# Kernel optimization log

Measured on AMD Instinct MI355X. Metric: run time of the kernel, lower is better.

The kernel has to match this reference:

```python
import jax, jax.numpy as jnp
import numpy as np

B = 512; S = 6; Q = 2            # meta-batch, n_way*k_shot, n_way*q_query
DIM = 64; IMG = 28; N_WAY = 2
HEADS = 4; HD = DIM // HEADS     # retrieval heads / head dim
EPS = 1e-5


def _pool_mat(inp, out):
    # exact torch AdaptiveAvgPool2d windowing as a matrix [out, inp]
    P = np.zeros((out, inp), np.float32)
    for i in range(out):
        s = (i * inp) // out
        e = -((-(i + 1) * inp) // out)
        P[i, s:e] = 1.0 / (e - s)
    return jnp.asarray(P)

P28 = _pool_mat(IMG, 8)  # 28 -> 8; subsequent 8 -> 8 pools are identity


def _gelu(x):
    return jax.nn.gelu(x, approximate=False)


def _conv(x, w, b):
    y = jax.lax.conv_general_dilated(x, w, (1, 1), ((1, 1), (1, 1)),
                                     dimension_numbers=('NCHW', 'OIHW', 'NCHW'))
    return y + b[None, :, None, None]


def _bn(x, p):
    # p rows: gamma, beta, running_mean, running_var (eval-mode BatchNorm2d)
    g, bt, m, v = p[0], p[1], p[2], p[3]
    sc = g / jnp.sqrt(v + EPS)
    return (x - m[None, :, None, None]) * sc[None, :, None, None] + bt[None, :, None, None]


def _img_in(x, c1w, c1b, bn1, c2w, c2b, bn2, c3w, c3b, bn3, c4w, c4b, bn4, lin_w):
    h = _bn(_conv(x, c1w, c1b), bn1)
    h = jnp.einsum('oi,ncij,pj->ncop', P28, h, P28)   # adaptive avg pool 28x28 -> 8x8
    h = _gelu(h)                                       # dropout is identity in eval
    h = _gelu(_bn(_conv(h, c2w, c2b), bn2))
    h = _gelu(_bn(_conv(h, c3w, c3b), bn3))
    h = _gelu(_bn(_conv(h, c4w, c4b), bn4))            # -> [N,1,8,8]
    h = h.reshape(h.shape[0], -1)                      # [N,64]
    return h @ lin_w.T                                 # Linear(64 -> DIM, no bias)


def _net(x, w1, w2):
    # x: [B,K,D]; w1,w2: [B,D,D] batched fast weights
    h = jnp.einsum('bed,bkd->bke', w1, x)
    ah = _gelu(h)
    y = jnp.einsum('bed,bkd->bke', w2, ah)
    return y, h


def _get_lor(x, w1, w2, r_q, r_k, r_v, r_o, ln_w, ln_b):
    b, k, _ = x.shape
    q, _ = _net(x, w1, w2)
    qh = jnp.einsum('nhd,bkd->bknh', r_q, q)
    sc = jnp.einsum('bknh,rnh->bknr', qh, r_k) / (HD ** 0.5)
    p = jax.nn.softmax(sc, axis=-1)
    lor = jnp.einsum('bknr,rnh->bknh', p, r_v).reshape(b, k, DIM)
    lor = jnp.einsum('de,bkd->bke', r_o, lor)
    z = lor + x
    mu = z.mean(-1, keepdims=True)
    var = ((z - mu) ** 2).mean(-1, keepdims=True)
    return (z - mu) / jnp.sqrt(var + EPS) * ln_w + ln_b


def _forward(query_w, sxs, qxs, inner_lr, c1w, c1b, bn1, c2w, c2b, bn2, c3w, c3b, bn3,
             c4w, c4b, bn4, lin_w, emb, w1, w2, tags, r_q, r_k, r_v, r_o, ln_w, ln_b,
             sys, qys):
    b = query_w.shape[0]
    s = sxs.shape[1]
    q = qxs.shape[1]
    feats = lambda im: _img_in(im.reshape(-1, 1, IMG, IMG), c1w, c1b, bn1, c2w, c2b,
                               bn2, c3w, c3b, bn3, c4w, c4b, bn4, lin_w)
    sx = feats(sxs).reshape(b, s, DIM)
    qx = feats(qxs).reshape(b, q, DIM)
    qe = tags[4]
    w1b = jnp.broadcast_to(w1, (b, DIM, DIM))
    w2b = jnp.broadcast_to(w2, (b, DIM, DIM))
    bound = sx + emb[sys]                                          # [B,S,D]
    # all 4 tag variants for all S shots in one vectorized get_lor call
    inp = (bound[:, :, None, :] + tags[:4][None, None]).reshape(b, s * 4, DIM)
    lors = _get_lor(inp, w1b, w2b, r_q, r_k, r_v, r_o, ln_w, ln_b).reshape(b, s, 4, DIM)
    l1s, r1s, l2s, r2s = lors[:, :, 0], lors[:, :, 1], lors[:, :, 2], lors[:, :, 3]
    qw1 = w1[None] + jnp.einsum('bsl,bsr->blr', l1s, r1s)
    qw2 = w2[None] + jnp.einsum('bsl,bsr->blr', l2s, r2s)
    preds, _ = _net(qx + qe, qw1, qw2)                             # [B,Q,D]
    logits = jnp.einsum('ld,bqd->bql', emb, preds).reshape(-1, N_WAY)
    labels = qys.reshape(-1)
    ls = jax.nn.log_softmax(logits)
    task_loss = -jnp.take_along_axis(ls, labels[:, None], axis=1).mean()
    n_correct = (jnp.argmax(logits, axis=1) == labels).sum()
    return task_loss, n_correct, b * q


def setup_inputs() -> dict:
    key = jax.random.key(0)
    ks = jax.random.split(key, 24)
    rn = lambda i, sh, sc=1.0: sc * jax.random.normal(ks[i], sh, jnp.float32)
    def bnp(i, c):
        k0, k1, k2 = jax.random.split(ks[i], 3)
        return jnp.stack([1.0 + 0.1 * jax.random.normal(k0, (c,)),
                          0.1 * jax.random.normal(k1, (c,)),
                          0.1 * jax.random.normal(k2, (c,)),
                          0.5 + jax.random.uniform(jax.random.fold_in(ks[i], 3), (c,))])
    return {
        'query_w': rn(0, (B, DIM)),
        'sxs': rn(1, (B, S, IMG * IMG)),
        'qxs': rn(2, (B, Q, IMG * IMG)),
        'inner_lr': jnp.float32(0.1),
        'c1w': rn(3, (32, 1, 3, 3), 0.3), 'c1b': rn(4, (32,), 0.1), 'bn1': bnp(5, 32),
        'c2w': rn(6, (32, 32, 3, 3), 0.06), 'c2b': rn(7, (32,), 0.1), 'bn2': bnp(8, 32),
        'c3w': rn(9, (32, 32, 3, 3), 0.06), 'c3b': rn(10, (32,), 0.1), 'bn3': bnp(11, 32),
        'c4w': rn(12, (1, 32, 3, 3), 0.06), 'c4b': rn(13, (1,), 0.1), 'bn4': bnp(14, 1),
        'lin_w': rn(15, (DIM, 64), 0.125),
        'emb': rn(16, (N_WAY, DIM), 0.125),
        'w1': rn(17, (DIM, DIM), 0.125),
        'w2': rn(18, (DIM, DIM), 0.125),
        'tags': rn(19, (8, DIM), 0.125),
        'r_q': rn(20, (HEADS, HD, DIM), 0.125),
        'r_k': rn(21, (16, HEADS, HD), 0.25),
        'r_v': rn(22, (16, HEADS, HD), 0.25),
        'r_o': rn(23, (DIM, DIM), 0.125),
        'ln_w': 0.001 * jnp.ones((DIM,), jnp.float32),
        'ln_b': jnp.zeros((DIM,), jnp.float32),
        'sys': jax.random.randint(jax.random.fold_in(key, 100), (B, S), 0, N_WAY),
        'qys': jax.random.randint(jax.random.fold_in(key, 101), (B, Q), 0, N_WAY),
    }


def reference(query_w, sxs, qxs, inner_lr, c1w, c1b, bn1, c2w, c2b, bn2, c3w, c3b, bn3,
              c4w, c4b, bn4, lin_w, emb, w1, w2, tags, r_q, r_k, r_v, r_o, ln_w, ln_b,
              sys, qys):
    task_loss, n_correct, n_q = _forward(query_w, sxs, qxs, inner_lr, c1w, c1b, bn1,
                                         c2w, c2b, bn2, c3w, c3b, bn3, c4w, c4b, bn4,
                                         lin_w, emb, w1, w2, tags, r_q, r_k, r_v, r_o,
                                         ln_w, ln_b, sys, qys)
    return (task_loss, task_loss, jnp.float32(0.0), n_correct, n_q)
```

## Files before the change

kernel.cpp:

```cpp
#include <hip/hip_runtime.h>
#include <math.h>

constexpr int NSUP = 3072;
constexpr float EPSF = 1e-5f;

constexpr int WS_W1B  = 0;
constexpr int WS_B1   = 1024;
constexpr int WS_W2B  = 1056;
constexpr int WS_W3B  = 5664;
constexpr int WS_W4B  = 10272;
constexpr int WS_B4   = 10416;
constexpr int WS_B2   = 10420;
constexpr int WS_B3   = 10452;
constexpr int WS_HW1  = 10484;
constexpr int WS_HW2  = 12788;
constexpr int WS_HRQ  = 15092;
constexpr int WS_HROT = 17396;
constexpr int WS_PART = 19700;
constexpr int WS_FEATS= 20724;

using short8 = __attribute__((ext_vector_type(8))) short;
using f32x4  = __attribute__((ext_vector_type(4))) float;

__device__ __forceinline__ float gelu_f(float x) {
    return 0.5f * x * (1.0f + erff(x * 0.70710678118654752440f));
}
__device__ __forceinline__ unsigned short f2bf(float f) {
    unsigned u = __float_as_uint(f);
    return (unsigned short)((u + 0x7FFFu + ((u >> 16) & 1u)) >> 16);
}
__device__ __forceinline__ float bflo(unsigned u) { return __uint_as_float(u << 16); }
__device__ __forceinline__ float bfhi(unsigned u) { return __uint_as_float(u & 0xffff0000u); }

__global__ void __launch_bounds__(256) precompute_kernel(
    const float* __restrict__ c1w, const float* __restrict__ c1b, const float* __restrict__ bn1,
    const float* __restrict__ c2w, const float* __restrict__ c2b, const float* __restrict__ bn2,
    const float* __restrict__ c3w, const float* __restrict__ c3b, const float* __restrict__ bn3,
    const float* __restrict__ c4w, const float* __restrict__ c4b, const float* __restrict__ bn4,
    const float* __restrict__ w1, const float* __restrict__ w2,
    const float* __restrict__ rq, const float* __restrict__ ro,
    float* __restrict__ ws)
{
    const int gid = blockIdx.x * 256 + threadIdx.x;
    const int gsz = gridDim.x * 256;

    unsigned short* w1b = (unsigned short*)(ws + WS_W1B);
    for (int v = gid; v < 2048; v += gsz) {
        int kt = v >> 10, rem = v & 1023, oc = rem >> 5, kk = rem & 31;
        int tap = kt * 32 + kk;
        unsigned short o = 0;
        if (tap < 36) {
            int tt = tap / 6, s = tap - tt * 6;
            float sum = 0.f;
            for (int di = 0; di < 3; ++di) {
                int a = tt - di; if (a < 0 || a > 3) continue;
                for (int dj = 0; dj < 3; ++dj) {
                    int bb = s - dj; if (bb < 0 || bb > 3) continue;
                    sum += c1w[oc * 9 + di * 3 + dj];
                }
            }
            float sc1 = bn1[oc] * rsqrtf(bn1[96 + oc] + EPSF);
            o = f2bf(sum * sc1 * (1.0f / 16.0f));
        }
        w1b[v] = o;
    }
    for (int c = gid; c < 32; c += gsz) {
        float sc1 = bn1[c] * rsqrtf(bn1[96 + c] + EPSF);
        ws[WS_B1 + c] = (c1b[c] - bn1[64 + c]) * sc1 + bn1[32 + c];
        float sc2 = bn2[c] * rsqrtf(bn2[96 + c] + EPSF);
        ws[WS_B2 + c] = (c2b[c] - bn2[64 + c]) * sc2 + bn2[32 + c];
        float sc3 = bn3[c] * rsqrtf(bn3[96 + c] + EPSF);
        ws[WS_B3 + c] = (c3b[c] - bn3[64 + c]) * sc3 + bn3[32 + c];
    }
    unsigned short* w2b = (unsigned short*)(ws + WS_W2B);
    unsigned short* w3b = (unsigned short*)(ws + WS_W3B);
    for (int v = gid; v < 9216; v += gsz) {
        int tap = v >> 10, oc = (v >> 5) & 31, ic = v & 31;
        float sc2 = bn2[oc] * rsqrtf(bn2[96 + oc] + EPSF);
        float sc3 = bn3[oc] * rsqrtf(bn3[96 + oc] + EPSF);
        w2b[v] = f2bf(c2w[oc * 288 + ic * 9 + tap] * sc2);
        w3b[v] = f2bf(c3w[oc * 288 + ic * 9 + tap] * sc3);
    }
    {
        unsigned short* w4b = (unsigned short*)(ws + WS_W4B);
        float sc4 = bn4[0] * rsqrtf(bn4[3] + EPSF);
        for (int v = gid; v < 288; v += gsz) {
            int tap = v >> 5, ic = v & 31;
            w4b[v] = f2bf(c4w[ic * 9 + tap] * sc4);
        }
        if (gid == 0) ws[WS_B4] = (c4b[0] - bn4[2]) * sc4 + bn4[1];
    }
    unsigned short* hw1 = (unsigned short*)(ws + WS_HW1);
    unsigned short* hw2 = (unsigned short*)(ws + WS_HW2);
    unsigned short* hrq = (unsigned short*)(ws + WS_HRQ);
    unsigned short* hro = (unsigned short*)(ws + WS_HROT);
    for (int v = gid; v < 4608; v += gsz) {
        int e = v / 72, d = v - e * 72;
        unsigned short a = 0, b = 0, c = 0, r = 0;
        if (d < 64) {
            a = f2bf(w1[e * 64 + d]);
            b = f2bf(w2[e * 64 + d]);
            c = f2bf(rq[e * 64 + d]);
            r = f2bf(ro[d * 64 + e]);
        }
        hw1[v] = a; hw2[v] = b; hrq[v] = c; hro[v] = r;
    }
}

__global__ void __launch_bounds__(512, 4) feats_kernel(
    const float* __restrict__ sxs, const float* __restrict__ qxs,
    const float* __restrict__ lin_w, const float* __restrict__ ws,
    float* __restrict__ feats)
{
    __shared__ __align__(16) unsigned short sAct[8][3200];
    __shared__ __align__(16) unsigned short sWB[9216];
    __shared__ __align__(16) float sh4[8][64];

    const int t    = threadIdx.x;
    const int wv   = t >> 6;
    const int lane = t & 63;
    const int col  = lane & 15;
    const int quad = lane >> 4;
    const int n    = blockIdx.x * 8 + wv;

    unsigned short* A = sAct[wv];

    {
        uint4 z = {0, 0, 0, 0};
        for (int i = t; i < 3200; i += 512) ((uint4*)sAct)[i] = z;
        if (t < 256) ((uint4*)sWB)[t] = ((const uint4*)(ws + WS_W1B))[t];
    }
    __syncthreads();

    {
        const float* img = (n < NSUP) ? (sxs + (size_t)n * 784) : (qxs + (size_t)(n - NSUP) * 784);
        int ttj[8], ssj[8];
        #pragma unroll
        for (int j = 0; j < 8; ++j) {
            int k = quad * 8 + j;
            ttj[j] = k / 6; ssj[j] = k - ttj[j] * 6;
        }
        f32x4 acc[4][2];
        #pragma unroll
        for (int mt = 0; mt < 4; ++mt) { acc[mt][0] = (f32x4){0,0,0,0}; acc[mt][1] = (f32x4){0,0,0,0}; }

        short8 b00 = *(const short8*)(sWB + (0 * 32 + 0 * 16 + col) * 32 + quad * 8);
        short8 b01 = *(const short8*)(sWB + (0 * 32 + 1 * 16 + col) * 32 + quad * 8);
        short8 b10 = *(const short8*)(sWB + (1 * 32 + 0 * 16 + col) * 32 + quad * 8);
        short8 b11 = *(const short8*)(sWB + (1 * 32 + 1 * 16 + col) * 32 + quad * 8);

        #pragma unroll
        for (int mt = 0; mt < 4; ++mt) {
            int px = mt * 16 + col;
            int sr = (((px >> 3) * 7) >> 1) - 1;
            int sc = (((px & 7) * 7) >> 1) - 1;
            short8 a0;
            #pragma unroll
            for (int j = 0; j < 8; ++j) {
                int rr = sr + ttj[j], cc = sc + ssj[j];
                float v = ((unsigned)rr < 28u && (unsigned)cc < 28u) ? img[rr * 28 + cc] : 0.f;
                a0[j] = (short)f2bf(v);
            }
            acc[mt][0] = __builtin_amdgcn_mfma_f32_16x16x32_bf16(a0, b00, acc[mt][0], 0, 0, 0);
            acc[mt][1] = __builtin_amdgcn_mfma_f32_16x16x32_bf16(a0, b01, acc[mt][1], 0, 0, 0);
            short8 a1 = {0,0,0,0,0,0,0,0};
            if (quad == 0) {
                #pragma unroll
                for (int j = 0; j < 4; ++j) {
                    int rr = sr + 5, cc = sc + 2 + j;
                    float v = ((unsigned)rr < 28u && (unsigned)cc < 28u) ? img[rr * 28 + cc] : 0.f;
                    a1[j] = (short)f2bf(v);
                }
            }
            acc[mt][0] = __builtin_amdgcn_mfma_f32_16x16x32_bf16(a1, b10, acc[mt][0], 0, 0, 0);
            acc[mt][1] = __builtin_amdgcn_mfma_f32_16x16x32_bf16(a1, b11, acc[mt][1], 0, 0, 0);
        }
        float bi0 = ws[WS_B1 + col], bi1 = ws[WS_B1 + 16 + col];
        #pragma unroll
        for (int mt = 0; mt < 4; ++mt)
            #pragma unroll
            for (int reg = 0; reg < 4; ++reg) {
                int px = mt * 16 + quad * 4 + reg;
                unsigned short* dst = A + (((px >> 3) + 1) * 10 + (px & 7) + 1) * 32;
                dst[col]      = f2bf(gelu_f(acc[mt][0][reg] + bi0));
                dst[col + 16] = f2bf(gelu_f(acc[mt][1][reg] + bi1));
            }
    }
    __syncthreads();
    for (int i = t; i < 1152; i += 512) ((uint4*)sWB)[i] = ((const uint4*)(ws + WS_W2B))[i];
    __syncthreads();

    #pragma unroll 1
    for (int layer = 0; layer < 2; ++layer) {
        f32x4 acc[4][2];
        #pragma unroll
        for (int mt = 0; mt < 4; ++mt) { acc[mt][0] = (f32x4){0,0,0,0}; acc[mt][1] = (f32x4){0,0,0,0}; }
        const unsigned short* abase[4];
        #pragma unroll
        for (int mt = 0; mt < 4; ++mt) {
            int px = mt * 16 + col;
            abase[mt] = A + ((px >> 3) * 10 + (px & 7)) * 32 + quad * 8;
        }
        #pragma unroll
        for (int dr = 0; dr < 3; ++dr)
            #pragma unroll
            for (int dc = 0; dc < 3; ++dc) {
                int tap = dr * 3 + dc;
                short8 b0 = *(const short8*)(sWB + (tap * 32 + col) * 32 + quad * 8);
                short8 b1 = *(const short8*)(sWB + (tap * 32 + 16 + col) * 32 + quad * 8);
                #pragma unroll
                for (int mt = 0; mt < 4; ++mt) {
                    short8 a = *(const short8*)(abase[mt] + (dr * 10 + dc) * 32);
                    acc[mt][0] = __builtin_amdgcn_mfma_f32_16x16x32_bf16(a, b0, acc[mt][0], 0, 0, 0);
                    acc[mt][1] = __builtin_amdgcn_mfma_f32_16x16x32_bf16(a, b1, acc[mt][1], 0, 0, 0);
                }
            }
        float bi0 = ws[(layer ? WS_B3 : WS_B2) + col];
        float bi1 = ws[(layer ? WS_B3 : WS_B2) + 16 + col];
        #pragma unroll
        for (int mt = 0; mt < 4; ++mt)
            #pragma unroll
            for (int reg = 0; reg < 4; ++reg) {
                int px = mt * 16 + quad * 4 + reg;
                unsigned short* dst = A + (((px >> 3) + 1) * 10 + (px & 7) + 1) * 32;
                dst[col]      = f2bf(gelu_f(acc[mt][0][reg] + bi0));
                dst[col + 16] = f2bf(gelu_f(acc[mt][1][reg] + bi1));
            }
        __syncthreads();
        if (layer == 0) {
            for (int i = t; i < 1152; i += 512) ((uint4*)sWB)[i] = ((const uint4*)(ws + WS_W3B))[i];
            __syncthreads();
        }
    }

    {
        f32x4 acc4[4];
        #pragma unroll
        for (int mt = 0; mt < 4; ++mt) acc4[mt] = (f32x4){0,0,0,0};
        const unsigned short* abase[4];
        #pragma unroll
        for (int mt = 0; mt < 4; ++mt) {
            int px = mt * 16 + col;
            abase[mt] = A + ((px >> 3) * 10 + (px & 7)) * 32 + quad * 8;
        }
        const unsigned short* w4g = (const unsigned short*)(ws + WS_W4B);
        #pragma unroll
        for (int dr = 0; dr < 3; ++dr)
            #pragma unroll
            for (int dc = 0; dc < 3; ++dc) {
                int tap = dr * 3 + dc;
                short8 b = *(const short8*)(w4g + tap * 32 + quad * 8);
                #pragma unroll
                for (int mt = 0; mt < 4; ++mt) {
                    short8 a = *(const short8*)(abase[mt] + (dr * 10 + dc) * 32);
                    acc4[mt] = __builtin_amdgcn_mfma_f32_16x16x32_bf16(a, b, acc4[mt], 0, 0, 0);
                }
            }
        if (col < 4) {
            f32x4 v = acc4[0];
            if (col == 1) v = acc4[1];
            else if (col == 2) v = acc4[2];
            else if (col == 3) v = acc4[3];
            float b4 = ws[WS_B4];
            #pragma unroll
            for (int reg = 0; reg < 4; ++reg)
                sh4[wv][col * 16 + quad * 4 + reg] = gelu_f(v[reg] + b4);
        }
    }
    __syncthreads();

    {
        const float4* lw = (const float4*)(lin_w + (size_t)lane * 64);
        const float4* hp = (const float4*)sh4[wv];
        float acc = 0.f;
        #pragma unroll
        for (int j = 0; j < 16; ++j) {
            float4 w = lw[j], h = hp[j];
            acc += w.x * h.x + w.y * h.y + w.z * h.z + w.w * h.w;
        }
        feats[n * 64 + lane] = acc;
    }
}

__device__ __forceinline__ void head_gemm(const unsigned short* __restrict__ Ab,
                                          const unsigned short* __restrict__ Bw,
                                          int col, int quad, int wvid, f32x4 res[2])
{
    #pragma unroll
    for (int u = 0; u < 2; ++u) {
        int tau = wvid + u * 4;
        int mt = tau & 1, nt = tau >> 1;
        f32x4 acc = {0, 0, 0, 0};
        #pragma unroll
        for (int kt = 0; kt < 2; ++kt) {
            short8 a = *(const short8*)(Ab + (mt * 16 + col) * 72 + kt * 32 + quad * 8);
            short8 b = *(const short8*)(Bw + (nt * 16 + col) * 72 + kt * 32 + quad * 8);
            acc = __builtin_amdgcn_mfma_f32_16x16x32_bf16(a, b, acc, 0, 0, 0);
        }
        res[u] = acc;
    }
}

__global__ void __launch_bounds__(256, 2) head_kernel(
    const float* __restrict__ emb, const float* __restrict__ tags,
    const float* __restrict__ rk, const float* __restrict__ rv,
    const float* __restrict__ lnw, const float* __restrict__ lnb,
    const int* __restrict__ sys, const int* __restrict__ qys,
    const float* __restrict__ ws, const float* __restrict__ feats,
    float* __restrict__ part)
{
    __shared__ __align__(16) unsigned short sW1B[4608], sW2B[4608], sRQB[4608], sROT[4608];
    __shared__ __align__(16) unsigned short bufA[2304], bufB[2304];
    __shared__ __align__(16) float sXf[1536];
    __shared__ __align__(16) float s_xq[128], s_ah[128], s_yp[128];
    __shared__ float s_t1[12], s_t2[12], s_mu[24], s_rs[24], s_lg[4];

    const int t    = threadIdx.x;
    const int b    = blockIdx.x;
    const int wvid = t >> 6;
    const int col  = t & 15;
    const int quad = (t >> 4) & 3;

    for (int i = t; i < 576; i += 256) {
        ((uint4*)sW1B)[i] = ((const uint4*)(ws + WS_HW1))[i];
        ((uint4*)sW2B)[i] = ((const uint4*)(ws + WS_HW2))[i];
        ((uint4*)sRQB)[i] = ((const uint4*)(ws + WS_HRQ))[i];
        ((uint4*)sROT)[i] = ((const uint4*)(ws + WS_HROT))[i];
    }
    if (t < 72) {
        uint4 z = {0, 0, 0, 0};
        ((uint4*)(bufA + 1728))[t] = z;
        ((uint4*)(bufB + 1728))[t] = z;
    }
    for (int idx = t; idx < 1536; idx += 256) {
        int k = idx >> 6, e = idx & 63;
        int s = k >> 2, tg = k & 3;
        int cls = sys[b * 6 + s];
        float v = feats[(b * 6 + s) * 64 + e] + emb[cls * 64 + e] + tags[tg * 64 + e];
        sXf[idx] = v;
        bufA[k * 72 + e] = f2bf(v);
    }
    __syncthreads();

    f32x4 r[2];
    head_gemm(bufA, sW1B, col, quad, wvid, r);
    #pragma unroll
    for (int u = 0; u < 2; ++u) {
        int tau = wvid + u * 4, mt = tau & 1, nt = tau >> 1;
        #pragma unroll
        for (int reg = 0; reg < 4; ++reg) {
            int row = mt * 16 + quad * 4 + reg;
            if (row < 24) bufB[row * 72 + nt * 16 + col] = f2bf(gelu_f(r[u][reg]));
        }
    }
    __syncthreads();
    head_gemm(bufB, sW2B, col, quad, wvid, r);
    #pragma unroll
    for (int u = 0; u < 2; ++u) {
        int tau = wvid + u * 4, mt = tau & 1, nt = tau >> 1;
        #pragma unroll
        for (int reg = 0; reg < 4; ++reg) {
            int row = mt * 16 + quad * 4 + reg;
            if (row < 24) bufA[row * 72 + nt * 16 + col] = f2bf(r[u][reg]);
        }
    }
    __syncthreads();
    head_gemm(bufA, sRQB, col, quad, wvid, r);
    #pragma unroll
    for (int u = 0; u < 2; ++u) {
        int tau = wvid + u * 4, mt = tau & 1, nt = tau >> 1;
        #pragma unroll
        for (int reg = 0; reg < 4; ++reg) {
            int row = mt * 16 + quad * 4 + reg;
            if (row < 24) bufB[row * 72 + nt * 16 + col] = f2bf(r[u][reg]);
        }
    }
    __syncthreads();

    if (t < 96) {
        int k = t >> 2, nn = t & 3;
        const unsigned short* qp = bufB + k * 72 + nn * 16;
        uint4 u0 = *(const uint4*)(qp);
        uint4 u1 = *(const uint4*)(qp + 8);
        float qv[16];
        qv[0]=bflo(u0.x); qv[1]=bfhi(u0.x); qv[2]=bflo(u0.y); qv[3]=bfhi(u0.y);
        qv[4]=bflo(u0.z); qv[5]=bfhi(u0.z); qv[6]=bflo(u0.w); qv[7]=bfhi(u0.w);
        qv[8]=bflo(u1.x); qv[9]=bfhi(u1.x); qv[10]=bflo(u1.y); qv[11]=bfhi(u1.y);
        qv[12]=bflo(u1.z); qv[13]=bfhi(u1.z); qv[14]=bflo(u1.w); qv[15]=bfhi(u1.w);
        float sc[16]; float mx = -1e30f;
        #pragma unroll
        for (int rr = 0; rr < 16; ++rr) {
            const float* kp = rk + rr * 64 + nn * 16;
            float d = 0.f;
            #pragma unroll
            for (int h = 0; h < 16; ++h) d += qv[h] * kp[h];
            d *= 0.25f;
            sc[rr] = d; mx = fmaxf(mx, d);
        }
        float sum = 0.f;
        #pragma unroll
        for (int rr = 0; rr < 16; ++rr) { sc[rr] = expf(sc[rr] - mx); sum += sc[rr]; }
        float inv = 1.0f / sum;
        float o[16];
        #pragma unroll
        for (int h = 0; h < 16; ++h) o[h] = 0.f;
        #pragma unroll
        for (int rr = 0; rr < 16; ++rr) {
            const float* vp = rv + rr * 64 + nn * 16;
            float p = sc[rr];
            #pragma unroll
            for (int h = 0; h < 16; ++h) o[h] += p * vp[h];
        }
        unsigned short* op = bufA + k * 72 + nn * 16;
        #pragma unroll
        for (int h = 0; h < 16; ++h) op[h] = f2bf(o[h] * inv);
    }
    __syncthreads();

    head_gemm(bufA, sROT, col, quad, wvid, r);
    #pragma unroll
    for (int u = 0; u < 2; ++u) {
        int tau = wvid + u * 4, mt = tau & 1, nt = tau >> 1;
        #pragma unroll
        for (int reg = 0; reg < 4; ++reg) {
            int row = mt * 16 + quad * 4 + reg;
            if (row < 24) {
                int idx = row * 64 + nt * 16 + col;
                sXf[idx] = sXf[idx] + r[u][reg];
            }
        }
    }
    __syncthreads();

    if (t < 24) {
        const float4* zp = (const float4*)(sXf + t * 64);
        float sx_ = 0.f;
        #pragma unroll
        for (int j = 0; j < 16; ++j) {
            float4 v = zp[(j + t) & 15];
            sx_ += v.x + v.y + v.z + v.w;
        }
        float mu = sx_ * (1.0f / 64.0f);
        float vv = 0.f;
        #pragma unroll
        for (int j = 0; j < 16; ++j) {
            float4 v = zp[(j + t) & 15];
            float d0 = v.x - mu, d1 = v.y - mu, d2 = v.z - mu, d3 = v.w - mu;
            vv += d0*d0 + d1*d1 + d2*d2 + d3*d3;
        }
        s_mu[t] = mu;
        s_rs[t] = 1.0f / sqrtf(vv * (1.0f / 64.0f) + EPSF);
    }
    __syncthreads();
    for (int idx = t; idx < 1536; idx += 256) {
        int k = idx >> 6, e = idx & 63;
        float v = (sXf[idx] - s_mu[k]) * s_rs[k] * lnw[e] + lnb[e];
        bufB[k * 72 + e] = f2bf(v);
    }
    if (t < 128) {
        int q = t >> 6, e = t & 63;
        s_xq[t] = feats[(NSUP + b * 2 + q) * 64 + e] + tags[256 + e];
    }
    __syncthreads();

    if (t < 12) {
        int q = t / 6, s = t - q * 6;
        const uint4* rp = (const uint4*)(bufB + (s * 4 + 1) * 72);
        const float* xp = s_xq + q * 64;
        float d = 0.f;
        #pragma unroll
        for (int j = 0; j < 8; ++j) {
            uint4 u = rp[j];
            const float* x = xp + j * 8;
            d += bflo(u.x)*x[0] + bfhi(u.x)*x[1] + bflo(u.y)*x[2] + bfhi(u.y)*x[3]
               + bflo(u.z)*x[4] + bfhi(u.z)*x[5] + bflo(u.w)*x[6] + bfhi(u.w)*x[7];
        }
        s_t1[t] = d;
    }
    __syncthreads();
    if (t < 128) {
        int q = t >> 6, e = t & 63;
        const uint4* wp = (const uint4*)(sW1B + e * 72);
        const float* xp = s_xq + q * 64;
        float acc = 0.f;
        #pragma unroll
        for (int j = 0; j < 8; ++j) {
            uint4 u = wp[j];
            const float* x = xp + j * 8;
            acc += bflo(u.x)*x[0] + bfhi(u.x)*x[1] + bflo(u.y)*x[2] + bfhi(u.y)*x[3]
                 + bflo(u.z)*x[4] + bfhi(u.z)*x[5] + bflo(u.w)*x[6] + bfhi(u.w)*x[7];
        }
        #pragma unroll
        for (int s = 0; s < 6; ++s)
            acc += bflo((unsigned)bufB[(s * 4 + 0) * 72 + e]) * s_t1[q * 6 + s];
        s_ah[t] = gelu_f(acc);
    }
    __syncthreads();
    if (t < 12) {
        int q = t / 6, s = t - q * 6;
        const uint4* rp = (const uint4*)(bufB + (s * 4 + 3) * 72);
        const float* xp = s_ah + q * 64;
        float d = 0.f;
        #pragma unroll
        for (int j = 0; j < 8; ++j) {
            uint4 u = rp[j];
            const float* x = xp + j * 8;
            d += bflo(u.x)*x[0] + bfhi(u.x)*x[1] + bflo(u.y)*x[2] + bfhi(u.y)*x[3]
               + bflo(u.z)*x[4] + bfhi(u.z)*x[5] + bflo(u.w)*x[6] + bfhi(u.w)*x[7];
        }
        s_t2[t] = d;
    }
    __syncthreads();
    if (t < 128) {
        int q = t >> 6, e = t & 63;
        const uint4* wp = (const uint4*)(sW2B + e * 72);
        const float* xp = s_ah + q * 64;
        float acc = 0.f;
        #pragma unroll
        for (int j = 0; j < 8; ++j) {
            uint4 u = wp[j];
            const float* x = xp + j * 8;
            acc += bflo(u.x)*x[0] + bfhi(u.x)*x[1] + bflo(u.y)*x[2] + bfhi(u.y)*x[3]
                 + bflo(u.z)*x[4] + bfhi(u.z)*x[5] + bflo(u.w)*x[6] + bfhi(u.w)*x[7];
        }
        #pragma unroll
        for (int s = 0; s < 6; ++s)
            acc += bflo((unsigned)bufB[(s * 4 + 2) * 72 + e]) * s_t2[q * 6 + s];
        s_yp[t] = acc;
    }
    __syncthreads();
    if (t < 4) {
        int q = t >> 1, ll = t & 1;
        const float4* ep = (const float4*)(emb + ll * 64);
        const float4* yp = (const float4*)(s_yp + q * 64);
        float d = 0.f;
        #pragma unroll
        for (int j = 0; j < 16; ++j) {
            float4 a = ep[j], x = yp[j];
            d += a.x*x.x + a.y*x.y + a.z*x.z + a.w*x.w;
        }
        s_lg[t] = d;
    }
    __syncthreads();
    if (t == 0) {
        float lsum = 0.f, corr = 0.f;
        #pragma unroll
        for (int q = 0; q < 2; ++q) {
            float l0 = s_lg[q * 2], l1 = s_lg[q * 2 + 1];
            int lab = qys[b * 2 + q];
            float m = fmaxf(l0, l1);
            float lse = m + logf(expf(l0 - m) + expf(l1 - m));
            lsum += -((lab ? l1 : l0) - lse);
            int pred = (l1 > l0) ? 1 : 0;
            corr += (pred == lab) ? 1.0f : 0.0f;
        }
        part[b] = lsum;
        part[512 + b] = corr;
    }
}

__global__ void __launch_bounds__(256) finalize_kernel(const float* __restrict__ part,
                                                       float* __restrict__ out)
{
    __shared__ float sl[256], sc[256];
    const int t = threadIdx.x;
    sl[t] = part[t] + part[t + 256];
    sc[t] = part[512 + t] + part[768 + t];
    __syncthreads();
    for (int s = 128; s > 0; s >>= 1) {
        if (t < s) { sl[t] += sl[t + s]; sc[t] += sc[t + s]; }
        __syncthreads();
    }
    if (t == 0) {
        float loss = sl[0] * (1.0f / 1024.0f);
        out[0] = loss;
        out[1] = loss;
        out[2] = 0.0f;
        out[3] = sc[0];
        out[4] = 1024.0f;
    }
}

extern "C" void kernel_launch(void* const* d_in, const int* in_sizes, int n_in,
                              void* d_out, int out_size, void* d_ws, size_t ws_size,
                              hipStream_t stream)
{
    (void)in_sizes; (void)n_in; (void)out_size; (void)ws_size;
    const float* sxs  = (const float*)d_in[1];
    const float* qxs  = (const float*)d_in[2];
    const float* c1w  = (const float*)d_in[4];
    const float* c1b  = (const float*)d_in[5];
    const float* bn1  = (const float*)d_in[6];
    const float* c2w  = (const float*)d_in[7];
    const float* c2b  = (const float*)d_in[8];
    const float* bn2  = (const float*)d_in[9];
    const float* c3w  = (const float*)d_in[10];
    const float* c3b  = (const float*)d_in[11];
    const float* bn3  = (const float*)d_in[12];
    const float* c4w  = (const float*)d_in[13];
    const float* c4b  = (const float*)d_in[14];
    const float* bn4  = (const float*)d_in[15];
    const float* lin_w= (const float*)d_in[16];
    const float* emb  = (const float*)d_in[17];
    const float* w1   = (const float*)d_in[18];
    const float* w2   = (const float*)d_in[19];
    const float* tags = (const float*)d_in[20];
    const float* rq   = (const float*)d_in[21];
    const float* rk   = (const float*)d_in[22];
    const float* rv   = (const float*)d_in[23];
    const float* ro   = (const float*)d_in[24];
    const float* lnw  = (const float*)d_in[25];
    const float* lnb  = (const float*)d_in[26];
    const int*   sys  = (const int*)d_in[27];
    const int*   qys  = (const int*)d_in[28];

    float* ws  = (float*)d_ws;
    float* out = (float*)d_out;

    precompute_kernel<<<64, 256, 0, stream>>>(c1w, c1b, bn1, c2w, c2b, bn2,
                                              c3w, c3b, bn3, c4w, c4b, bn4,
                                              w1, w2, rq, ro, ws);
    feats_kernel<<<512, 512, 0, stream>>>(sxs, qxs, lin_w, ws, ws + WS_FEATS);
    head_kernel<<<512, 256, 0, stream>>>(emb, tags, rk, rv, lnw, lnb, sys, qys,
                                         ws, ws + WS_FEATS, ws + WS_PART);
    finalize_kernel<<<1, 256, 0, stream>>>(ws + WS_PART, out);
}
```

Baseline: 174.1 us.

## Read conv and head weights from global memory instead of staging them in LDS

Both feats and head kernels stop copying weight matrices into shared memory and read the MFMA B-operands straight from global (L2/L1-cached) memory. This removes the staging copies and most block-wide barriers, so each wavefront in feats runs independently. Feats blocks shrink to 4 waves with twice as many blocks, and head's occupancy hint is raised. The cost is repeated global/L1 loads of the weights per wave, which can add latency where LDS reads used to be.

Result: no change. 175.7 us (+0.9%).

```diff
diff --git a/kernel.cpp b/kernel.cpp
--- a/kernel.cpp
+++ b/kernel.cpp
@@ -107,32 +107,30 @@
     }
 }
 
-__global__ void __launch_bounds__(512, 4) feats_kernel(
+__global__ void __launch_bounds__(256, 4) feats_kernel(
     const float* __restrict__ sxs, const float* __restrict__ qxs,
     const float* __restrict__ lin_w, const float* __restrict__ ws,
     float* __restrict__ feats)
 {
-    __shared__ __align__(16) unsigned short sAct[8][3200];
-    __shared__ __align__(16) unsigned short sWB[9216];
-    __shared__ __align__(16) float sh4[8][64];
+    __shared__ __align__(16) unsigned short sAct[4][3200];
+    __shared__ __align__(16) float sh4[4][64];
 
     const int t    = threadIdx.x;
     const int wv   = t >> 6;
     const int lane = t & 63;
     const int col  = lane & 15;
     const int quad = lane >> 4;
-    const int n    = blockIdx.x * 8 + wv;
+    const int n    = blockIdx.x * 4 + wv;
 
     unsigned short* A = sAct[wv];
 
     {
         uint4 z = {0, 0, 0, 0};
-        for (int i = t; i < 3200; i += 512) ((uint4*)sAct)[i] = z;
-        if (t < 256) ((uint4*)sWB)[t] = ((const uint4*)(ws + WS_W1B))[t];
-    }
-    __syncthreads();
+        for (int i = lane; i < 400; i += 64) ((uint4*)A)[i] = z;
+    }
 
     {
+        const unsigned short* w1b = (const unsigned short*)(ws + WS_W1B);
         const float* img = (n < NSUP) ? (sxs + (size_t)n * 784) : (qxs + (size_t)(n - NSUP) * 784);
         int ttj[8], ssj[8];
         #pragma unroll
@@ -144,10 +142,10 @@
         #pragma unroll
         for (int mt = 0; mt < 4; ++mt) { acc[mt][0] = (f32x4){0,0,0,0}; acc[mt][1] = (f32x4){0,0,0,0}; }
 
-        short8 b00 = *(const short8*)(sWB + (0 * 32 + 0 * 16 + col) * 32 + quad * 8);
-        short8 b01 = *(const short8*)(sWB + (0 * 32 + 1 * 16 + col) * 32 + quad * 8);
-        short8 b10 = *(const short8*)(sWB + (1 * 32 + 0 * 16 + col) * 32 + quad * 8);
-        short8 b11 = *(const short8*)(sWB + (1 * 32 + 1 * 16 + col) * 32 + quad * 8);
+        short8 b00 = *(const short8*)(w1b + (0 * 16 + col) * 32 + quad * 8);
+        short8 b01 = *(const short8*)(w1b + (1 * 16 + col) * 32 + quad * 8);
+        short8 b10 = *(const short8*)(w1b + 1024 + (0 * 16 + col) * 32 + quad * 8);
+        short8 b11 = *(const short8*)(w1b + 1024 + (1 * 16 + col) * 32 + quad * 8);
 
         #pragma unroll
         for (int mt = 0; mt < 4; ++mt) {
@@ -186,12 +184,10 @@
                 dst[col + 16] = f2bf(gelu_f(acc[mt][1][reg] + bi1));
             }
     }
-    __syncthreads();
-    for (int i = t; i < 1152; i += 512) ((uint4*)sWB)[i] = ((const uint4*)(ws + WS_W2B))[i];
-    __syncthreads();
 
     #pragma unroll 1
     for (int layer = 0; layer < 2; ++layer) {
+        const unsigned short* wb = (const unsigned short*)(ws + (layer ? WS_W3B : WS_W2B));
         f32x4 acc[4][2];
         #pragma unroll
         for (int mt = 0; mt < 4; ++mt) { acc[mt][0] = (f32x4){0,0,0,0}; acc[mt][1] = (f32x4){0,0,0,0}; }
@@ -206,8 +202,8 @@
             #pragma unroll
             for (int dc = 0; dc < 3; ++dc) {
                 int tap = dr * 3 + dc;
-                short8 b0 = *(const short8*)(sWB + (tap * 32 + col) * 32 + quad * 8);
-                short8 b1 = *(const short8*)(sWB + (tap * 32 + 16 + col) * 32 + quad * 8);
+                short8 b0 = *(const short8*)(wb + (tap * 32 + col) * 32 + quad * 8);
+                short8 b1 = *(const short8*)(wb + (tap * 32 + 16 + col) * 32 + quad * 8);
                 #pragma unroll
                 for (int mt = 0; mt < 4; ++mt) {
                     short8 a = *(const short8*)(abase[mt] + (dr * 10 + dc) * 32);
@@ -226,11 +222,6 @@
                 dst[col]      = f2bf(gelu_f(acc[mt][0][reg] + bi0));
                 dst[col + 16] = f2bf(gelu_f(acc[mt][1][reg] + bi1));
             }
-        __syncthreads();
-        if (layer == 0) {
-            for (int i = t; i < 1152; i += 512) ((uint4*)sWB)[i] = ((const uint4*)(ws + WS_W3B))[i];
-            __syncthreads();
-        }
     }
 
     {
@@ -267,7 +258,6 @@
                 sh4[wv][col * 16 + quad * 4 + reg] = gelu_f(v[reg] + b4);
         }
     }
-    __syncthreads();
 
     {
         const float4* lw = (const float4*)(lin_w + (size_t)lane * 64);
@@ -301,7 +291,7 @@
     }
 }
 
-__global__ void __launch_bounds__(256, 2) head_kernel(
+__global__ void __launch_bounds__(256, 4) head_kernel(
     const float* __restrict__ emb, const float* __restrict__ tags,
     const float* __restrict__ rk, const float* __restrict__ rv,
     const float* __restrict__ lnw, const float* __restrict__ lnb,
@@ -309,7 +299,6 @@
     const float* __restrict__ ws, const float* __restrict__ feats,
     float* __restrict__ part)
 {
-    __shared__ __align__(16) unsigned short sW1B[4608], sW2B[4608], sRQB[4608], sROT[4608];
     __shared__ __align__(16) unsigned short bufA[2304], bufB[2304];
     __shared__ __align__(16) float sXf[1536];
     __shared__ __align__(16) float s_xq[128], s_ah[128], s_yp[128];
@@ -321,12 +310,11 @@
     const int col  = t & 15;
     const int quad = (t >> 4) & 3;
 
-    for (int i = t; i < 576; i += 256) {
-        ((uint4*)sW1B)[i] = ((const uint4*)(ws + WS_HW1))[i];
-        ((uint4*)sW2B)[i] = ((const uint4*)(ws + WS_HW2))[i];
-        ((uint4*)sRQB)[i] = ((const uint4*)(ws + WS_HRQ))[i];
-        ((uint4*)sROT)[i] = ((const uint4*)(ws + WS_HROT))[i];
-    }
+    const unsigned short* W1g = (const unsigned short*)(ws + WS_HW1);
+    const unsigned short* W2g = (const unsigned short*)(ws + WS_HW2);
+    const unsigned short* RQg = (const unsigned short*)(ws + WS_HRQ);
+    const unsigned short* ROg = (const unsigned short*)(ws + WS_HROT);
+
     if (t < 72) {
         uint4 z = {0, 0, 0, 0};
         ((uint4*)(bufA + 1728))[t] = z;
@@ -343,7 +331,7 @@
     __syncthreads();
 
     f32x4 r[2];
-    head_gemm(bufA, sW1B, col, quad, wvid, r);
+    head_gemm(bufA, W1g, col, quad, wvid, r);
     #pragma unroll
     for (int u = 0; u < 2; ++u) {
         int tau = wvid + u * 4, mt = tau & 1, nt = tau >> 1;
@@ -354,7 +342,7 @@
         }
     }
     __syncthreads();
-    head_gemm(bufB, sW2B, col, quad, wvid, r);
+    head_gemm(bufB, W2g, col, quad, wvid, r);
     #pragma unroll
     for (int u = 0; u < 2; ++u) {
         int tau = wvid + u * 4, mt = tau & 1, nt = tau >> 1;
@@ -365,7 +353,7 @@
         }
     }
     __syncthreads();
-    head_gemm(bufA, sRQB, col, quad, wvid, r);
+    head_gemm(bufA, RQg, col, quad, wvid, r);
     #pragma unroll
     for (int u = 0; u < 2; ++u) {
         int tau = wvid + u * 4, mt = tau & 1, nt = tau >> 1;
@@ -417,7 +405,7 @@
     }
     __syncthreads();
 
-    head_gemm(bufA, sROT, col, quad, wvid, r);
+    head_gemm(bufA, ROg, col, quad, wvid, r);
     #pragma unroll
     for (int u = 0; u < 2; ++u) {
         int tau = wvid + u * 4, mt = tau & 1, nt = tau >> 1;
@@ -480,7 +468,7 @@
     __syncthreads();
     if (t < 128) {
         int q = t >> 6, e = t & 63;
-        const uint4* wp = (const uint4*)(sW1B + e * 72);
+        const uint4* wp = (const uint4*)(W1g + e * 72);
         const float* xp = s_xq + q * 64;
         float acc = 0.f;
         #pragma unroll
@@ -513,7 +501,7 @@
     __syncthreads();
     if (t < 128) {
         int q = t >> 6, e = t & 63;
-        const uint4* wp = (const uint4*)(sW2B + e * 72);
+        const uint4* wp = (const uint4*)(W2g + e * 72);
         const float* xp = s_ah + q * 64;
         float acc = 0.f;
         #pragma unroll
@@ -620,7 +608,7 @@
     precompute_kernel<<<64, 256, 0, stream>>>(c1w, c1b, bn1, c2w, c2b, bn2,
                                               c3w, c3b, bn3, c4w, c4b, bn4,
                                               w1, w2, rq, ro, ws);
-    feats_kernel<<<512, 512, 0, stream>>>(sxs, qxs, lin_w, ws, ws + WS_FEATS);
+    feats_kernel<<<1024, 256, 0, stream>>>(sxs, qxs, lin_w, ws, ws + WS_FEATS);
     head_kernel<<<512, 256, 0, stream>>>(emb, tags, rk, rv, lnw, lnb, sys, qys,
                                          ws, ws + WS_FEATS, ws + WS_PART);
     finalize_kernel<<<1, 256, 0, stream>>>(ws + WS_PART, out);
```
